# Kernel optimization log

Hardware: AMD Instinct MI355X
Metric: run time of the kernel (lower is better)

Reference implementation:

```python
import jax, jax.numpy as jnp
import numpy as np
from jax import lax

DN = ('NHWC', 'HWIO', 'NHWC')  # conv dimension numbers


def setup_inputs() -> dict:
    key = jax.random.key(0)
    ks = jax.random.split(key, 10)
    B, H, W, C, F, E = 16, 32, 32, 128, 128, 8
    G = F * (H // 2) * (W // 2)  # 32768, gating flatten size
    return {
        'x': jax.random.normal(ks[0], (B, H, W, C), jnp.float32),
        'eps_kernel': jax.random.normal(ks[1], (3, 3, C, F, E), jnp.float32),
        'eps_gate': jax.random.normal(ks[2], (B, E), jnp.float32),
        'expert_mu': jax.random.normal(ks[3], (3, 3, C, F, E), jnp.float32) * 0.05,
        'expert_rho': jax.random.normal(ks[4], (3, C, F, E), jnp.float32) * 0.01 - 6.0,
        'expert_bias': jax.random.normal(ks[5], (F, E), jnp.float32) * 0.01,
        'gating_kernel': jax.random.normal(ks[6], (3, 3, C, F), jnp.float32) * 0.05,
        'gating_bias': jax.random.normal(ks[7], (F,), jnp.float32) * 0.01,
        'gating_out_kernel': jax.random.normal(ks[8], (G, E), jnp.float32) * 0.01,
        'gating_out_bias': jax.random.normal(ks[9], (E,), jnp.float32) * 0.01,
    }


def reference(x, eps_kernel, eps_gate, expert_mu, expert_rho, expert_bias,
              gating_kernel, gating_bias, gating_out_kernel, gating_out_bias):
    GATING_NOISE_SIGMA = 1e-4
    TOP_K = 2
    B = x.shape[0]
    kh, kw, C, F, E = expert_mu.shape

    # Bayesian reparameterized expert kernels: rho shared over first kernel dim
    sigma = jax.nn.softplus(expert_rho)[None]               # [1,kw,C,F,E]
    kernel = expert_mu + sigma * eps_kernel                 # [kh,kw,C,F,E]

    # All-expert conv as one grouped conv via output-channel packing
    kern_flat = kernel.reshape(kh, kw, C, F * E)
    expert_out = lax.conv_general_dilated(x, kern_flat, (1, 1), 'SAME',
                                          dimension_numbers=DN)
    expert_out = expert_out.reshape(B, x.shape[1], x.shape[2], F, E)
    expert_out = expert_out + expert_bias                   # [B,H,W,F,E]

    # Gating path: conv -> 2x2 maxpool -> flatten -> dense -> noisy logits
    g = lax.conv_general_dilated(x, gating_kernel, (1, 1), 'SAME',
                                 dimension_numbers=DN) + gating_bias
    g = lax.reduce_window(g, -jnp.inf, lax.max,
                          (1, 2, 2, 1), (1, 2, 2, 1), 'VALID')
    logits = g.reshape(B, -1) @ gating_out_kernel + gating_out_bias  # [B,E]
    logits = logits + GATING_NOISE_SIGMA * eps_gate

    # noisy top-k gating: softmax over selected experts, zero elsewhere
    top_vals, top_idx = lax.top_k(logits, TOP_K)
    top_w = jax.nn.softmax(top_vals, axis=-1)
    gates = jnp.zeros((B, E), logits.dtype).at[
        jnp.arange(B)[:, None], top_idx].set(top_w)

    # combine experts weighted by gates, broadcast over spatial dims
    out = jnp.einsum('bhwfe,be->bhwf', expert_out, gates)
    return out
```

## Files before the change

### kernel.cpp

```cpp
#include <hip/hip_runtime.h>
#include <cmath>

#define B_ 16
#define H_ 32
#define W_ 32
#define C_ 128
#define F_ 128
#define KSZ (9*C_*F_)
#define NKS 36
#define FRAG_ELE 4096

typedef __bf16 bf16;
typedef __bf16 bf16x4 __attribute__((ext_vector_type(4)));
typedef __bf16 bf16x8 __attribute__((ext_vector_type(8)));
typedef float  f32x4  __attribute__((ext_vector_type(4)));

__device__ __forceinline__ float softplus_f(float v) {
  return log1pf(expf(-fabsf(v))) + fmaxf(v, 0.f);
}

__device__ __forceinline__ float logit_f(const float* part, const float* gob,
                                         const float* epsg, int bb, int e) {
  float s = 0.f;
  #pragma unroll
  for (int hb = 0; hb < 16; ++hb) s += part[(bb*16 + hb)*8 + e];
  return s + gob[e] + 1e-4f * epsg[bb*8 + e];
}

__device__ __forceinline__ void block_map_f(int bid, int* b, int* hb) {
  *b  = (bid & 7) * 2 + (bid >> 7);
  *hb = (bid >> 3) & 15;
}

template<int MODE>
__global__ __launch_bounds__(1024, 4) void conv_k(
    const float* __restrict__ x,
    const bf16* __restrict__ Bhi,
    const bf16* __restrict__ Blo,
    const float* __restrict__ gb,
    const float* __restrict__ Wg,
    const float* __restrict__ part,
    const float* __restrict__ gob,
    const float* __restrict__ epsg,
    const float* __restrict__ ebias,
    float* __restrict__ outv)
{
  int b, hb;
  block_map_f(blockIdx.x, &b, &hb);
  const int t   = threadIdx.x;
  const int l   = t & 63;
  const int wid = t >> 6;
  const int kg  = wid >> 3;
  const int w8  = wid & 7;

  __shared__ bf16 xs[MODE*4*34*128];
  __shared__ float red[8][8];
  __shared__ float gl8[8];
  __shared__ float gw2[2];
  __shared__ int   eid2[2];

  for (int v = t; v < 4*34*32; v += 1024) {
    int c4   = v & 31;
    int col  = (v >> 5) % 34;
    int rowi = (v >> 5) / 34;
    int row  = hb*2 - 1 + rowi;
    int w    = col - 1;
    float4 xv = make_float4(0.f, 0.f, 0.f, 0.f);
    if (row >= 0 && row < H_ && w >= 0 && w < W_)
      xv = *(const float4*)&x[((b*H_ + row)*W_ + w)*C_ + c4*4];
    float vv[4] = {xv.x, xv.y, xv.z, xv.w};
    bf16x4 h4, l4;
    #pragma unroll
    for (int j = 0; j < 4; ++j) {
      h4[j] = (bf16)vv[j];
      if (MODE == 2) l4[j] = (bf16)(vv[j] - (float)h4[j]);
    }
    int base = ((rowi*34 + col)*256 + c4*8) ^ ((col & 7) << 4);
    *(bf16x4*)((char*)xs + base) = h4;
    if (MODE == 2) *(bf16x4*)((char*)xs + 34816 + base) = l4;
  }
  if (MODE == 1 && t == 0) {
    float lg[8];
    #pragma unroll
    for (int e = 0; e < 8; ++e) lg[e] = logit_f(part, gob, epsg, b, e);
    int i0 = 0;
    #pragma unroll
    for (int e = 1; e < 8; ++e) if (lg[e] > lg[i0]) i0 = e;
    int i1 = (i0 == 0) ? 1 : 0;
    #pragma unroll
    for (int e = 0; e < 8; ++e) if (e != i0 && lg[e] > lg[i1]) i1 = e;
    float m  = fmaxf(lg[i0], lg[i1]);
    float e0 = expf(lg[i0] - m), e1 = expf(lg[i1] - m);
    float s  = e0 + e1;
    #pragma unroll
    for (int e = 0; e < 8; ++e) gl8[e] = 0.f;
    gl8[i0] = e0 / s;  gl8[i1] = e1 / s;
    eid2[0] = i0;      eid2[1] = i1;
    gw2[0]  = e0 / s;  gw2[1]  = e1 / s;
  }
  __syncthreads();

  const int mpar = w8 & 1;
  const int nf0  = (w8 >> 1) << 1;
  const int r15  = l & 15;
  const int q    = l >> 4;

  f32x4 acc00 = {0.f,0.f,0.f,0.f}, acc01 = acc00, acc10 = acc00, acc11 = acc00;
  f32x4 acd00 = acc00, acd01 = acc00, acd10 = acc00, acd11 = acc00;

  const bf16* B0;
  const bf16* B1;
  if (MODE == 1) { B0 = Bhi + (size_t)eid2[0]*KSZ; B1 = Bhi + (size_t)eid2[1]*KSZ; }
  else           { B0 = Bhi;                       B1 = Blo; }
  const size_t bgo = (size_t)(nf0*512 + l*8);

  bf16x8 s0h0,s0h1,s0l0,s0l1, s1h0,s1h1,s1l0,s1l1, s2h0,s2h1,s2l0,s2l1;

#define LOADB(S, KS_) do {                                                  \
    int kk_ = (KS_); if (kk_ > NKS-1) kk_ = NKS-1;                          \
    size_t o_ = bgo + (size_t)kk_ * FRAG_ELE;                               \
    S##h0 = *(const bf16x8*)(B0 + o_);                                      \
    S##h1 = *(const bf16x8*)(B0 + o_ + 512);                                \
    S##l0 = *(const bf16x8*)(B1 + o_);                                      \
    S##l1 = *(const bf16x8*)(B1 + o_ + 512);                                \
  } while (0)

#define MFMA16(a, bb_, c) __builtin_amdgcn_mfma_f32_16x16x32_bf16(a, bb_, c, 0, 0, 0)

#define COMPUTE(S, KS_) do {                                                \
    const int khkw_ = (KS_) >> 2;                                           \
    const int kh_ = khkw_ / 3, kw_ = khkw_ % 3;                             \
    const int c0_ = ((KS_) & 3) << 5;                                       \
    const int col_ = mpar*16 + r15 + kw_;                                   \
    const int off_ = ((kh_*34 + col_)*256 + (c0_ + q*8)*2) ^ ((col_ & 7) << 4); \
    bf16x8 a0_ = *(const bf16x8*)((const char*)xs + off_);                  \
    bf16x8 a1_ = *(const bf16x8*)((const char*)xs + off_ + 8704);           \
    __builtin_amdgcn_s_setprio(1);                                          \
    acc00 = MFMA16(a0_, S##h0, acc00);                                      \
    acc01 = MFMA16(a0_, S##h1, acc01);                                      \
    acc10 = MFMA16(a1_, S##h0, acc10);                                      \
    acc11 = MFMA16(a1_, S##h1, acc11);                                      \
    if (MODE == 2) {                                                        \
      bf16x8 g0_ = *(const bf16x8*)((const char*)xs + 34816 + off_);        \
      bf16x8 g1_ = *(const bf16x8*)((const char*)xs + 34816 + off_ + 8704); \
      acc00 = MFMA16(g0_, S##h0, acc00);                                    \
      acc01 = MFMA16(g0_, S##h1, acc01);                                    \
      acc10 = MFMA16(g1_, S##h0, acc10);                                    \
      acc11 = MFMA16(g1_, S##h1, acc11);                                    \
      acc00 = MFMA16(a0_, S##l0, acc00);                                    \
      acc01 = MFMA16(a0_, S##l1, acc01);                                    \
      acc10 = MFMA16(a1_, S##l0, acc10);                                    \
      acc11 = MFMA16(a1_, S##l1, acc11);                                    \
    } else {                                                                \
      acd00 = MFMA16(a0_, S##l0, acd00);                                    \
      acd01 = MFMA16(a0_, S##l1, acd01);                                    \
      acd10 = MFMA16(a1_, S##l0, acd10);                                    \
      acd11 = MFMA16(a1_, S##l1, acd11);                                    \
    }                                                                       \
    __builtin_amdgcn_s_setprio(0);                                          \
  } while (0)

  const int ks0 = kg * (NKS/2);
  LOADB(s0, ks0); LOADB(s1, ks0+1); LOADB(s2, ks0+2);
  for (int ks = ks0; ks < ks0 + NKS/2; ks += 3) {
    COMPUTE(s0, ks);   LOADB(s0, ks+3);
    COMPUTE(s1, ks+1); LOADB(s1, ks+4);
    COMPUTE(s2, ks+2); LOADB(s2, ks+5);
  }
#undef LOADB
#undef COMPUTE

  if (MODE == 1) {
    const float g0 = gw2[0], g1 = gw2[1];
    #pragma unroll
    for (int r = 0; r < 4; ++r) {
      acc00[r] = g0*acc00[r] + g1*acd00[r];
      acc01[r] = g0*acc01[r] + g1*acd01[r];
      acc10[r] = g0*acc10[r] + g1*acd10[r];
      acc11[r] = g0*acc11[r] + g1*acd11[r];
    }
  }

  __syncthreads();
  float* comb = (float*)xs;
  if (kg == 1) {
    #pragma unroll
    for (int r = 0; r < 4; ++r) {
      comb[(w8*16 + 0  + r)*64 + l] = acc00[r];
      comb[(w8*16 + 4  + r)*64 + l] = acc01[r];
      comb[(w8*16 + 8  + r)*64 + l] = acc10[r];
      comb[(w8*16 + 12 + r)*64 + l] = acc11[r];
    }
  }
  __syncthreads();
  if (kg == 0) {
    #pragma unroll
    for (int r = 0; r < 4; ++r) {
      acc00[r] += comb[(w8*16 + 0  + r)*64 + l];
      acc01[r] += comb[(w8*16 + 4  + r)*64 + l];
      acc10[r] += comb[(w8*16 + 8  + r)*64 + l];
      acc11[r] += comb[(w8*16 + 12 + r)*64 + l];
    }
  }

  if (MODE == 1) {
    if (kg == 0) {
      const int f0 = nf0*16 + r15;
      float bv0 = 0.f, bv1 = 0.f;
      #pragma unroll
      for (int e = 0; e < 8; ++e) {
        bv0 += gl8[e] * ebias[f0*8 + e];
        bv1 += gl8[e] * ebias[(f0+16)*8 + e];
      }
      #pragma unroll
      for (int mi = 0; mi < 2; ++mi) {
        const int h = hb*2 + mi;
        #pragma unroll
        for (int r = 0; r < 4; ++r) {
          const int wo = mpar*16 + q*4 + r;
          float* o = &outv[((b*H_ + h)*W_ + wo)*F_];
          o[f0]      = (mi ? acc10[r] : acc00[r]) + bv0;
          o[f0 + 16] = (mi ? acc11[r] : acc01[r]) + bv1;
        }
      }
    }
  } else {
    float pr[8] = {0,0,0,0,0,0,0,0};
    if (kg == 0) {
      #pragma unroll
      for (int ni = 0; ni < 2; ++ni) {
        const int f = (nf0 + ni)*16 + r15;
        const float bv = gb[f];
        #pragma unroll
        for (int pp = 0; pp < 2; ++pp) {
          float m0 = ni ? fmaxf(acc01[2*pp], acc01[2*pp+1])
                        : fmaxf(acc00[2*pp], acc00[2*pp+1]);
          float m1 = ni ? fmaxf(acc11[2*pp], acc11[2*pp+1])
                        : fmaxf(acc10[2*pp], acc10[2*pp+1]);
          float pm = fmaxf(m0, m1) + bv;
          const int pw = mpar*8 + q*2 + pp;
          const float* wr = &Wg[(size_t)((hb*16 + pw)*128 + f) * 8];
          float4 wA = *(const float4*)wr;
          float4 wB = *(const float4*)(wr + 4);
          pr[0] += pm*wA.x; pr[1] += pm*wA.y; pr[2] += pm*wA.z; pr[3] += pm*wA.w;
          pr[4] += pm*wB.x; pr[5] += pm*wB.y; pr[6] += pm*wB.z; pr[7] += pm*wB.w;
        }
      }
    }
    #pragma unroll
    for (int o = 32; o > 0; o >>= 1)
      #pragma unroll
      for (int e = 0; e < 8; ++e) pr[e] += __shfl_down(pr[e], o);
    if (l == 0 && kg == 0)
      #pragma unroll
      for (int e = 0; e < 8; ++e) red[w8][e] = pr[e];
    __syncthreads();
    if (t < 8) {
      float s = 0.f;
      #pragma unroll
      for (int w = 0; w < 8; ++w) s += red[w][t];
      outv[(b*16 + hb)*8 + t] = s;
    }
  }
}

__global__ __launch_bounds__(256) void prep_k(
    const float* __restrict__ mu, const float* __restrict__ rho,
    const float* __restrict__ eps, const float* __restrict__ gk,
    bf16* __restrict__ bank, bf16* __restrict__ bgh, bf16* __restrict__ bgl)
{
  __shared__ float tile[32*129];
  const int bid = blockIdx.x;
  const int t   = threadIdx.x;

  if (bid < 2*NKS) {
    const int ks = bid >> 1;
    const int nf = (bid & 1)*4 + (t >> 6);
    const int l  = t & 63;
    const int khkw = ks >> 2;
    const int kw   = khkw % 3;
    const int f    = nf*16 + (l & 15);
    const int cb   = (ks & 3)*32 + (l >> 4)*8;

    bf16x8 ob[8];
    #pragma unroll
    for (int j = 0; j < 8; ++j) {
      const int c = cb + j;
      const float* mp = &mu [(size_t)((khkw*C_ + c)*F_ + f) * 8];
      const float* ep = &eps[(size_t)((khkw*C_ + c)*F_ + f) * 8];
      const float* rp = &rho[(size_t)((kw  *C_ + c)*F_ + f) * 8];
      #pragma unroll
      for (int e = 0; e < 8; ++e)
        ob[e][j] = (bf16)(mp[e] + softplus_f(rp[e]) * ep[e]);
    }
    #pragma unroll
    for (int e = 0; e < 8; ++e) {
      size_t o = (size_t)e*KSZ + (size_t)ks*FRAG_ELE + nf*512 + l*8;
      *(bf16x8*)&bank[o] = ob[e];
    }
  } else {
    const int ks   = bid - 2*NKS;
    const int khkw = ks >> 2;
    const int cb   = (ks & 3)*32;
    for (int v = t; v < 1024; v += 256) {
      int c  = v >> 5;
      int f4 = (v & 31) * 4;
      float4 val = *(const float4*)&gk[(size_t)(khkw*C_ + cb + c)*F_ + f4];
      float* dst = &tile[c*129 + f4];
      dst[0] = val.x; dst[1] = val.y; dst[2] = val.z; dst[3] = val.w;
    }
    __syncthreads();
    for (int tt = t; tt < 512; tt += 256) {
      const int nf = tt >> 6, l = tt & 63;
      const int f  = nf*16 + (l & 15);
      bf16x8 h8, l8;
      #pragma unroll
      for (int j = 0; j < 8; ++j) {
        int c = (l >> 4)*8 + j;
        float v = tile[c*129 + f];
        bf16 h = (bf16)v;
        h8[j] = h;
        l8[j] = (bf16)(v - (float)h);
      }
      *(bf16x8*)&bgh[(size_t)ks*FRAG_ELE + tt*8] = h8;
      *(bf16x8*)&bgl[(size_t)ks*FRAG_ELE + tt*8] = l8;
    }
  }
}

extern "C" void kernel_launch(void* const* d_in, const int* in_sizes, int n_in,
                              void* d_out, int out_size, void* d_ws, size_t ws_size,
                              hipStream_t stream) {
  const float* x    = (const float*)d_in[0];
  const float* epsk = (const float*)d_in[1];
  const float* epsg = (const float*)d_in[2];
  const float* mu   = (const float*)d_in[3];
  const float* rho  = (const float*)d_in[4];
  const float* ebias= (const float*)d_in[5];
  const float* gk   = (const float*)d_in[6];
  const float* gb   = (const float*)d_in[7];
  const float* gok  = (const float*)d_in[8];
  const float* gob  = (const float*)d_in[9];
  float* out = (float*)d_out;

  char* ws = (char*)d_ws;
  bf16*  bank = (bf16*) (ws);
  bf16*  bgh  = (bf16*) (ws + 2359296);
  bf16*  bgl  = (bf16*) (ws + 2654208);
  float* part = (float*)(ws + 2949120);

  prep_k<<<3*NKS, 256, 0, stream>>>(mu, rho, epsk, gk, bank, bgh, bgl);
  conv_k<2><<<B_*16, 1024, 0, stream>>>(x, bgh, bgl, gb, gok,
                                        nullptr, nullptr, nullptr, nullptr, part);
  conv_k<1><<<B_*16, 1024, 0, stream>>>(x, bank, nullptr, nullptr, nullptr,
                                        part, gob, epsg, ebias, out);
}
```

Before: 55.62 us.

## Overlap expert kernel sampling with gating conv by folding into extra blocks

After: 54.85 us. Within noise of the previous version (-1.4%).

```diff
diff --git a/kernel.cpp b/kernel.cpp
--- a/kernel.cpp
+++ b/kernel.cpp
@@ -43,12 +43,44 @@
     const float* __restrict__ gob,
     const float* __restrict__ epsg,
     const float* __restrict__ ebias,
+    const float* __restrict__ mu,
+    const float* __restrict__ rho,
+    const float* __restrict__ epsk,
+    bf16* __restrict__ bank,
     float* __restrict__ outv)
 {
-  int b, hb;
-  block_map_f(blockIdx.x, &b, &hb);
   const int t   = threadIdx.x;
   const int l   = t & 63;
+
+  if (MODE == 2 && blockIdx.x < NKS) {
+    if (t < 512) {
+      const int ks = blockIdx.x;
+      const int nf = t >> 6;
+      const int khkw = ks >> 2, kw = khkw % 3;
+      const int f  = nf*16 + (l & 15);
+      const int cb = (ks & 3)*32 + (l >> 4)*8;
+      bf16x8 ob[8];
+      #pragma unroll
+      for (int j = 0; j < 8; ++j) {
+        const int c = cb + j;
+        const float* mp = &mu  [(size_t)((khkw*C_ + c)*F_ + f) * 8];
+        const float* ep = &epsk[(size_t)((khkw*C_ + c)*F_ + f) * 8];
+        const float* rp = &rho [(size_t)((kw  *C_ + c)*F_ + f) * 8];
+        #pragma unroll
+        for (int e = 0; e < 8; ++e)
+          ob[e][j] = (bf16)(mp[e] + softplus_f(rp[e]) * ep[e]);
+      }
+      #pragma unroll
+      for (int e = 0; e < 8; ++e) {
+        size_t o = (size_t)e*KSZ + (size_t)ks*FRAG_ELE + nf*512 + l*8;
+        *(bf16x8*)&bank[o] = ob[e];
+      }
+    }
+    return;
+  }
+
+  int b, hb;
+  block_map_f(MODE == 2 ? blockIdx.x - NKS : blockIdx.x, &b, &hb);
   const int wid = t >> 6;
   const int kg  = wid >> 3;
   const int w8  = wid & 7;
@@ -264,67 +296,38 @@
   }
 }
 
-__global__ __launch_bounds__(256) void prep_k(
-    const float* __restrict__ mu, const float* __restrict__ rho,
-    const float* __restrict__ eps, const float* __restrict__ gk,
-    bf16* __restrict__ bank, bf16* __restrict__ bgh, bf16* __restrict__ bgl)
+__global__ __launch_bounds__(1024) void gkprep_k(
+    const float* __restrict__ gk, bf16* __restrict__ bgh, bf16* __restrict__ bgl)
 {
   __shared__ float tile[32*129];
-  const int bid = blockIdx.x;
-  const int t   = threadIdx.x;
-
-  if (bid < 2*NKS) {
-    const int ks = bid >> 1;
-    const int nf = (bid & 1)*4 + (t >> 6);
-    const int l  = t & 63;
-    const int khkw = ks >> 2;
-    const int kw   = khkw % 3;
-    const int f    = nf*16 + (l & 15);
-    const int cb   = (ks & 3)*32 + (l >> 4)*8;
-
-    bf16x8 ob[8];
+  const int ks   = blockIdx.x;
+  const int khkw = ks >> 2;
+  const int cb   = (ks & 3)*32;
+  const int t    = threadIdx.x;
+
+  {
+    int c  = t >> 5;
+    int f4 = (t & 31) * 4;
+    float4 val = *(const float4*)&gk[(size_t)(khkw*C_ + cb + c)*F_ + f4];
+    float* dst = &tile[c*129 + f4];
+    dst[0] = val.x; dst[1] = val.y; dst[2] = val.z; dst[3] = val.w;
+  }
+  __syncthreads();
+
+  if (t < 512) {
+    const int nf = t >> 6, l = t & 63;
+    const int f  = nf*16 + (l & 15);
+    bf16x8 h8, l8;
     #pragma unroll
     for (int j = 0; j < 8; ++j) {
-      const int c = cb + j;
-      const float* mp = &mu [(size_t)((khkw*C_ + c)*F_ + f) * 8];
-      const float* ep = &eps[(size_t)((khkw*C_ + c)*F_ + f) * 8];
-      const float* rp = &rho[(size_t)((kw  *C_ + c)*F_ + f) * 8];
-      #pragma unroll
-      for (int e = 0; e < 8; ++e)
-        ob[e][j] = (bf16)(mp[e] + softplus_f(rp[e]) * ep[e]);
-    }
-    #pragma unroll
-    for (int e = 0; e < 8; ++e) {
-      size_t o = (size_t)e*KSZ + (size_t)ks*FRAG_ELE + nf*512 + l*8;
-      *(bf16x8*)&bank[o] = ob[e];
-    }
-  } else {
-    const int ks   = bid - 2*NKS;
-    const int khkw = ks >> 2;
-    const int cb   = (ks & 3)*32;
-    for (int v = t; v < 1024; v += 256) {
-      int c  = v >> 5;
-      int f4 = (v & 31) * 4;
-      float4 val = *(const float4*)&gk[(size_t)(khkw*C_ + cb + c)*F_ + f4];
-      float* dst = &tile[c*129 + f4];
-      dst[0] = val.x; dst[1] = val.y; dst[2] = val.z; dst[3] = val.w;
-    }
-    __syncthreads();
-    for (int tt = t; tt < 512; tt += 256) {
-      const int nf = tt >> 6, l = tt & 63;
-      const int f  = nf*16 + (l & 15);
-      bf16x8 h8, l8;
-      #pragma unroll
-      for (int j = 0; j < 8; ++j) {
-        int c = (l >> 4)*8 + j;
-        float v = tile[c*129 + f];
-        bf16 h = (bf16)v;
-        h8[j] = h;
-        l8[j] = (bf16)(v - (float)h);
-      }
-      *(bf16x8*)&bgh[(size_t)ks*FRAG_ELE + tt*8] = h8;
-      *(bf16x8*)&bgl[(size_t)ks*FRAG_ELE + tt*8] = l8;
-    }
+      int c = (l >> 4)*8 + j;
+      float v = tile[c*129 + f];
+      bf16 h = (bf16)v;
+      h8[j] = h;
+      l8[j] = (bf16)(v - (float)h);
+    }
+    *(bf16x8*)&bgh[(size_t)ks*FRAG_ELE + t*8] = h8;
+    *(bf16x8*)&bgl[(size_t)ks*FRAG_ELE + t*8] = l8;
   }
 }
 
@@ -349,9 +352,11 @@
   bf16*  bgl  = (bf16*) (ws + 2654208);
   float* part = (float*)(ws + 2949120);
 
-  prep_k<<<3*NKS, 256, 0, stream>>>(mu, rho, epsk, gk, bank, bgh, bgl);
-  conv_k<2><<<B_*16, 1024, 0, stream>>>(x, bgh, bgl, gb, gok,
-                                        nullptr, nullptr, nullptr, nullptr, part);
-  conv_k<1><<<B_*16, 1024, 0, stream>>>(x, bank, nullptr, nullptr, nullptr,
-                                        part, gob, epsg, ebias, out);
-}
+  gkprep_k<<<NKS, 1024, 0, stream>>>(gk, bgh, bgl);
+  conv_k<2><<<NKS + 256, 1024, 0, stream>>>(x, bgh, bgl, gb, gok,
+                                            nullptr, nullptr, nullptr, nullptr,
+                                            mu, rho, epsk, bank, part);
+  conv_k<1><<<256, 1024, 0, stream>>>(x, bank, nullptr, nullptr, nullptr,
+                                      part, gob, epsg, ebias,
+                                      nullptr, nullptr, nullptr, nullptr, out);
+}
```
